# Kernel tuning notes

Measured on AMD Instinct MI355X. Metric: run time of the kernel, lower is better.

Reference implementation:

```python
import jax, jax.numpy as jnp
import numpy as np

# GCN ('gcn' variant): avg-pooled adjacency, per-step linear + propagation + ReLU,
# final output projection, then select the target (first) node of each block.
# The original builds a dense block-diagonal (B*n, B*n) adjacency via torch.block_diag;
# since off-block entries are exactly zero, this is mathematically identical to
# batched per-block matmuls, which is what we do here.

B, N_NODES, D_IN, D_HID, D_OUT, STEPS = 256, 512, 256, 256, 128, 3


def setup_inputs() -> dict:
    key = jax.random.key(0)
    ks = jax.random.split(key, 6)
    xavier = lambda k, shp: jax.random.normal(k, shp, jnp.float32) * np.sqrt(2.0 / (shp[0] + shp[1]))
    feat = jax.random.normal(ks[0], (B * N_NODES, D_IN), jnp.float32)
    raw_adj = jax.random.uniform(ks[1], (B, N_NODES, N_NODES), jnp.float32)
    W0 = xavier(ks[2], (D_IN, D_HID))
    W1 = xavier(ks[3], (D_HID, D_HID))
    W2 = xavier(ks[4], (D_HID, D_HID))
    Wout = xavier(ks[5], (D_HID, D_OUT))
    return {"feat": feat, "raw_adj": raw_adj, "W0": W0, "W1": W1, "W2": W2, "Wout": Wout}


def reference(feat, raw_adj, W0, W1, W2, Wout):
    b, n, _ = raw_adj.shape
    d = feat.shape[1]
    Xb = feat.reshape(b, n, d)  # block view of feat

    # avg_pooling: row-normalize adjacency by the sum over columns whose
    # feature rows are nonzero (block-diagonal => per-block computation).
    nz = (jnp.linalg.norm(Xb, axis=2) > 0).astype(raw_adj.dtype)  # (b, n)
    row_sum = jnp.einsum('bij,bj->bi', raw_adj, nz)               # (b, n)
    row_sum = jnp.where(row_sum == 0, 1.0, row_sum)
    adj = raw_adj / row_sum[:, :, None]

    X = Xb
    for W in (W0, W1, W2):
        Z = jnp.einsum('bnd,dh->bnh', X, W)      # per-step linear (no bias)
        X = jax.nn.relu(jnp.einsum('bij,bjh->bih', adj, Z))  # propagate + ReLU
    out = jnp.einsum('bnh,ho->bno', X, Wout)     # output layer
    # X[ids] with ids = [0, n, 2n, ...] == first node of each block
    return out[:, 0, :]
```

## Files before the change

### kernel.cpp

```cpp
#include <hip/hip_runtime.h>


typedef __attribute__((ext_vector_type(8))) short short8;
typedef __attribute__((ext_vector_type(4))) float f32x4;

__device__ __forceinline__ unsigned short f2bf(float x) {
  unsigned u = __float_as_uint(x);
  unsigned r = u + 0x7fffu + ((u >> 16) & 1u);
  return (unsigned short)(r >> 16);
}
__device__ __forceinline__ float bf2f(unsigned short b) {
  return __uint_as_float(((unsigned)b) << 16);
}

#define GLDS(g, l) __builtin_amdgcn_global_load_lds( \
    (const __attribute__((address_space(1))) void*)(g), \
    (__attribute__((address_space(3))) void*)(l), 16, 0, 0)

__global__ void k_feat(const float* __restrict__ feat,
                       unsigned short* __restrict__ Xb,
                       float* __restrict__ nz) {
  int row = blockIdx.x * 4 + (threadIdx.x >> 6);
  int lane = threadIdx.x & 63;
  float4 v = ((const float4*)feat)[(size_t)row * 64 + lane];
  float ssq = v.x * v.x + v.y * v.y + v.z * v.z + v.w * v.w;
#pragma unroll
  for (int off = 1; off < 64; off <<= 1) ssq += __shfl_xor(ssq, off);
  if (lane == 0) nz[row] = (ssq > 0.f) ? 1.f : 0.f;
  ushort4 p;
  p.x = f2bf(v.x); p.y = f2bf(v.y); p.z = f2bf(v.z); p.w = f2bf(v.w);
  ((ushort4*)Xb)[(size_t)row * 64 + lane] = p;
}

__global__ void k_adj(const float* __restrict__ adj, const float* __restrict__ nz,
                      unsigned short* __restrict__ adjN) {
  int row = blockIdx.x * 4 + (threadIdx.x >> 6);
  int lane = threadIdx.x & 63;
  int b = row >> 9;
  const float4* src = (const float4*)(adj + (size_t)row * 512);
  float4 a0 = src[lane * 2], a1 = src[lane * 2 + 1];
  const float4* nzp = (const float4*)(nz + (size_t)b * 512);
  float4 z0 = nzp[lane * 2], z1 = nzp[lane * 2 + 1];
  float s = a0.x * z0.x + a0.y * z0.y + a0.z * z0.z + a0.w * z0.w
          + a1.x * z1.x + a1.y * z1.y + a1.z * z1.z + a1.w * z1.w;
#pragma unroll
  for (int off = 1; off < 64; off <<= 1) s += __shfl_xor(s, off);
  float inv = 1.f / ((s == 0.f) ? 1.f : s);
  uint4 p;
  p.x = (unsigned)f2bf(a0.x * inv) | ((unsigned)f2bf(a0.y * inv) << 16);
  p.y = (unsigned)f2bf(a0.z * inv) | ((unsigned)f2bf(a0.w * inv) << 16);
  p.z = (unsigned)f2bf(a1.x * inv) | ((unsigned)f2bf(a1.y * inv) << 16);
  p.w = (unsigned)f2bf(a1.z * inv) | ((unsigned)f2bf(a1.w * inv) << 16);
  ((uint4*)(adjN + (size_t)row * 512))[lane] = p;
}

__global__ void k_wconv(const float* __restrict__ W0, const float* __restrict__ W1,
                        unsigned short* __restrict__ Wt) {
  int s = blockIdx.x >> 8;
  int n = blockIdx.x & 255;
  int k = threadIdx.x;
  const float* W = s ? W1 : W0;
  Wt[(size_t)s * 65536 + n * 256 + k] = f2bf(W[(size_t)k * 256 + n]);
}

__device__ __forceinline__ void gemm_tile(
    const char* Ag, int ldaB, const char* Bg, int ldbB, int nkt,
    char* ldsA, char* ldsB, f32x4 acc[4][4], int wm, int wn, int lane, int tid) {
  for (int kt = 0; kt < nkt; ++kt) {
#pragma unroll
    for (int q = 0; q < 4; ++q) {
      int P = (q * 256 + tid) * 16;
      int L = P ^ (((P >> 7) & 7) << 4);
      int row = L >> 7, cb = L & 127;
      GLDS(Ag + (size_t)row * ldaB + kt * 128 + cb, ldsA + P);
      GLDS(Bg + (size_t)row * ldbB + kt * 128 + cb, ldsB + P);
    }
    __syncthreads();
#pragma unroll
    for (int ks = 0; ks < 2; ++ks) {
      short8 af[4], bfr[4];
      int c = ks * 64 + ((lane >> 4) << 4);
#pragma unroll
      for (int m = 0; m < 4; ++m) {
        int row = wm * 64 + m * 16 + (lane & 15);
        af[m] = *(const short8*)(ldsA + ((row * 128 + c) ^ ((row & 7) << 4)));
      }
#pragma unroll
      for (int n = 0; n < 4; ++n) {
        int row = wn * 64 + n * 16 + (lane & 15);
        bfr[n] = *(const short8*)(ldsB + ((row * 128 + c) ^ ((row & 7) << 4)));
      }
#pragma unroll
      for (int m = 0; m < 4; ++m)
#pragma unroll
        for (int n = 0; n < 4; ++n)
          acc[m][n] = __builtin_amdgcn_mfma_f32_16x16x32_bf16(af[m], bfr[n], acc[m][n], 0, 0, 0);
    }
    __syncthreads();
  }
}

__device__ __forceinline__ int swz2048(int bid) {
  return (bid & 7) * 256 + (bid >> 3);
}

__global__ __launch_bounds__(256) void k_linear(const unsigned short* __restrict__ X,
                                                const unsigned short* __restrict__ Wt,
                                                unsigned short* __restrict__ Zt) {
  __shared__ char lds[32768];
  int tid = threadIdx.x, lane = tid & 63, wid = tid >> 6;
  int wm = wid >> 1, wn = wid & 1;
  int tile = swz2048(blockIdx.x);
  int tm = tile >> 1, tn = tile & 1;
  const char* Ag = (const char*)(X + (size_t)tm * 128 * 256);
  const char* Bg = (const char*)(Wt + (size_t)tn * 128 * 256);
  f32x4 acc[4][4];
#pragma unroll
  for (int m = 0; m < 4; ++m)
#pragma unroll
    for (int n = 0; n < 4; ++n) { f32x4 z = {0.f, 0.f, 0.f, 0.f}; acc[m][n] = z; }
  gemm_tile(Ag, 512, Bg, 512, 4, lds, lds + 16384, acc, wm, wn, lane, tid);
  int b = tm >> 2;
  int node_base = ((tm & 3) * 128) + wm * 64;
  int h_base = tn * 128 + wn * 64;
#pragma unroll
  for (int m = 0; m < 4; ++m) {
    int node = node_base + m * 16 + ((lane >> 4) << 2);
#pragma unroll
    for (int n = 0; n < 4; ++n) {
      int h = h_base + n * 16 + (lane & 15);
      f32x4 v = acc[m][n];
      ushort4 p;
      p.x = f2bf(v[0]); p.y = f2bf(v[1]); p.z = f2bf(v[2]); p.w = f2bf(v[3]);
      *(ushort4*)(Zt + ((size_t)b * 256 + h) * 512 + node) = p;
    }
  }
}

__global__ __launch_bounds__(256) void k_prop(const unsigned short* __restrict__ adjN,
                                              const unsigned short* __restrict__ Zt,
                                              unsigned short* __restrict__ Xout) {
  __shared__ char lds[32768];
  int tid = threadIdx.x, lane = tid & 63, wid = tid >> 6;
  int wm = wid >> 1, wn = wid & 1;
  int tile = swz2048(blockIdx.x);
  int b = tile >> 3, tm = (tile >> 1) & 3, tn = tile & 1;
  const char* Ag = (const char*)(adjN + ((size_t)b * 512 + tm * 128) * 512);
  const char* Bg = (const char*)(Zt + ((size_t)b * 256 + tn * 128) * 512);
  f32x4 acc[4][4];
#pragma unroll
  for (int m = 0; m < 4; ++m)
#pragma unroll
    for (int n = 0; n < 4; ++n) { f32x4 z = {0.f, 0.f, 0.f, 0.f}; acc[m][n] = z; }
  gemm_tile(Ag, 1024, Bg, 1024, 8, lds, lds + 16384, acc, wm, wn, lane, tid);
  int node_base = tm * 128 + wm * 64;
  int h_base = tn * 128 + wn * 64;
#pragma unroll
  for (int m = 0; m < 4; ++m) {
    int node = node_base + m * 16 + ((lane >> 4) << 2);
#pragma unroll
    for (int n = 0; n < 4; ++n) {
      int h = h_base + n * 16 + (lane & 15);
#pragma unroll
      for (int r = 0; r < 4; ++r) {
        float v = acc[m][n][r];
        v = v > 0.f ? v : 0.f;
        Xout[((size_t)b * 512 + node + r) * 256 + h] = f2bf(v);
      }
    }
  }
}

__global__ __launch_bounds__(256) void k_tail(const unsigned short* __restrict__ adjN,
                                              const unsigned short* __restrict__ X2,
                                              const float* __restrict__ W2,
                                              const float* __restrict__ Wout,
                                              float* __restrict__ out) {
  __shared__ float aL[512];
  __shared__ float yL[8][256];
  __shared__ float y[256];
  __shared__ float x3[256];
  int b = blockIdx.x, tid = threadIdx.x;
  {
    const unsigned short* a0 = adjN + (size_t)b * 512 * 512;
    ushort2 v = ((const ushort2*)a0)[tid];
    aL[tid * 2] = bf2f(v.x);
    aL[tid * 2 + 1] = bf2f(v.y);
  }
  __syncthreads();
  {
    int hg = tid & 31, jg = tid >> 5;
    float acc[8] = {0.f, 0.f, 0.f, 0.f, 0.f, 0.f, 0.f, 0.f};
    const unsigned short* Xb = X2 + (size_t)b * 512 * 256;
    for (int jj = 0; jj < 64; ++jj) {
      int j = jj * 8 + jg;
      short8 xv = *(const short8*)(Xb + (size_t)j * 256 + hg * 8);
      float a = aL[j];
#pragma unroll
      for (int r = 0; r < 8; ++r) acc[r] += a * bf2f((unsigned short)xv[r]);
    }
#pragma unroll
    for (int r = 0; r < 8; ++r) yL[jg][hg * 8 + r] = acc[r];
  }
  __syncthreads();
  {
    float s = 0.f;
#pragma unroll
    for (int g = 0; g < 8; ++g) s += yL[g][tid];
    y[tid] = s;
  }
  __syncthreads();
  {
    float s = 0.f;
    for (int k = 0; k < 256; ++k) s += y[k] * W2[(size_t)k * 256 + tid];
    x3[tid] = s > 0.f ? s : 0.f;
  }
  __syncthreads();
  if (tid < 128) {
    float s = 0.f;
    for (int h = 0; h < 256; ++h) s += x3[h] * Wout[(size_t)h * 128 + tid];
    out[(size_t)b * 128 + tid] = s;
  }
}

extern "C" void kernel_launch(void* const* d_in, const int* in_sizes, int n_in,
                              void* d_out, int out_size, void* d_ws, size_t ws_size,
                              hipStream_t stream) {
  (void)in_sizes; (void)n_in; (void)out_size; (void)ws_size;
  const float* feat = (const float*)d_in[0];
  const float* adj  = (const float*)d_in[1];
  const float* W0   = (const float*)d_in[2];
  const float* W1   = (const float*)d_in[3];
  const float* W2   = (const float*)d_in[4];
  const float* Wout = (const float*)d_in[5];
  float* out = (float*)d_out;

  char* ws = (char*)d_ws;
  unsigned short* adjN = (unsigned short*)(ws);
  unsigned short* Xbuf = (unsigned short*)(ws + 134217728);
  unsigned short* Zt   = (unsigned short*)(ws + 201326592);
  float* nzbuf         = (float*)(ws + 268435456);
  unsigned short* Wt   = (unsigned short*)(ws + 268959744);

  k_feat<<<32768, 256, 0, stream>>>(feat, Xbuf, nzbuf);
  k_adj<<<32768, 256, 0, stream>>>(adj, nzbuf, adjN);
  k_wconv<<<512, 256, 0, stream>>>(W0, W1, Wt);

  k_linear<<<2048, 256, 0, stream>>>(Xbuf, Wt, Zt);
  k_prop<<<2048, 256, 0, stream>>>(adjN, Zt, Xbuf);
  k_linear<<<2048, 256, 0, stream>>>(Xbuf, Wt + 65536, Zt);
  k_prop<<<2048, 256, 0, stream>>>(adjN, Zt, Xbuf);
  k_tail<<<256, 256, 0, stream>>>(adjN, Xbuf, W2, Wout, out);
}
```

Measured before the change: 347.5 us.

## Fuse feature/adjacency conversion into GEMMs and compute row sums via MFMA

Removes the separate feat and adjacency preprocessing kernels. The first linear layer now reads fp32 features directly, converts them to bf16 in registers and writes the nonzero mask as a side output. The propagation kernel reads raw fp32 adjacency, converts it on the fly and computes row sums with an extra MFMA against the bf16 nz vector, applying the normalization in the epilogue. The bf16 adjN buffer write and re-read go away, but the fp32 adjacency (twice the bytes of bf16) is now read on each of the two propagation passes and in the tail, and A-tile loads become synchronous register loads instead of async global-to-LDS copies.

```diff
diff --git a/kernel.cpp b/kernel.cpp
--- a/kernel.cpp
+++ b/kernel.cpp
@@ -12,46 +12,18 @@
 __device__ __forceinline__ float bf2f(unsigned short b) {
   return __uint_as_float(((unsigned)b) << 16);
 }
+__device__ __forceinline__ unsigned pkbf(float lo, float hi) {
+  unsigned r;
+  asm("v_cvt_pk_bf16_f32 %0, %1, %2" : "=v"(r) : "v"(lo), "v"(hi));
+  return r;
+}
 
 #define GLDS(g, l) __builtin_amdgcn_global_load_lds( \
     (const __attribute__((address_space(1))) void*)(g), \
     (__attribute__((address_space(3))) void*)(l), 16, 0, 0)
 
-__global__ void k_feat(const float* __restrict__ feat,
-                       unsigned short* __restrict__ Xb,
-                       float* __restrict__ nz) {
-  int row = blockIdx.x * 4 + (threadIdx.x >> 6);
-  int lane = threadIdx.x & 63;
-  float4 v = ((const float4*)feat)[(size_t)row * 64 + lane];
-  float ssq = v.x * v.x + v.y * v.y + v.z * v.z + v.w * v.w;
-#pragma unroll
-  for (int off = 1; off < 64; off <<= 1) ssq += __shfl_xor(ssq, off);
-  if (lane == 0) nz[row] = (ssq > 0.f) ? 1.f : 0.f;
-  ushort4 p;
-  p.x = f2bf(v.x); p.y = f2bf(v.y); p.z = f2bf(v.z); p.w = f2bf(v.w);
-  ((ushort4*)Xb)[(size_t)row * 64 + lane] = p;
-}
-
-__global__ void k_adj(const float* __restrict__ adj, const float* __restrict__ nz,
-                      unsigned short* __restrict__ adjN) {
-  int row = blockIdx.x * 4 + (threadIdx.x >> 6);
-  int lane = threadIdx.x & 63;
-  int b = row >> 9;
-  const float4* src = (const float4*)(adj + (size_t)row * 512);
-  float4 a0 = src[lane * 2], a1 = src[lane * 2 + 1];
-  const float4* nzp = (const float4*)(nz + (size_t)b * 512);
-  float4 z0 = nzp[lane * 2], z1 = nzp[lane * 2 + 1];
-  float s = a0.x * z0.x + a0.y * z0.y + a0.z * z0.z + a0.w * z0.w
-          + a1.x * z1.x + a1.y * z1.y + a1.z * z1.z + a1.w * z1.w;
-#pragma unroll
-  for (int off = 1; off < 64; off <<= 1) s += __shfl_xor(s, off);
-  float inv = 1.f / ((s == 0.f) ? 1.f : s);
-  uint4 p;
-  p.x = (unsigned)f2bf(a0.x * inv) | ((unsigned)f2bf(a0.y * inv) << 16);
-  p.y = (unsigned)f2bf(a0.z * inv) | ((unsigned)f2bf(a0.w * inv) << 16);
-  p.z = (unsigned)f2bf(a1.x * inv) | ((unsigned)f2bf(a1.y * inv) << 16);
-  p.w = (unsigned)f2bf(a1.z * inv) | ((unsigned)f2bf(a1.w * inv) << 16);
-  ((uint4*)(adjN + (size_t)row * 512))[lane] = p;
+__device__ __forceinline__ int swz2048(int bid) {
+  return (bid & 7) * 256 + (bid >> 3);
 }
 
 __global__ void k_wconv(const float* __restrict__ W0, const float* __restrict__ W1,
@@ -100,8 +72,195 @@
   }
 }
 
-__device__ __forceinline__ int swz2048(int bid) {
-  return (bid & 7) * 256 + (bid >> 3);
+__global__ __launch_bounds__(256) void k_lin0(const float* __restrict__ feat,
+                                              const unsigned short* __restrict__ Wt,
+                                              unsigned short* __restrict__ Zt,
+                                              float* __restrict__ nzOut) {
+  __shared__ char ldsA[16384];
+  __shared__ char ldsB[16384];
+  int tid = threadIdx.x, lane = tid & 63, wid = tid >> 6;
+  int wm = wid >> 1, wn = wid & 1;
+  int tile = swz2048(blockIdx.x);
+  int tm = tile >> 1, tn = tile & 1;
+  const float* Ag = feat + (size_t)tm * 128 * 256;
+  const char* Bg = (const char*)(Wt + (size_t)tn * 128 * 256);
+  int r = tid >> 1, hk = tid & 1;
+  const float* myrow = Ag + (size_t)r * 256 + hk * 32;
+  float ssq = 0.f;
+  f32x4 acc[4][4];
+#pragma unroll
+  for (int m = 0; m < 4; ++m)
+#pragma unroll
+    for (int n = 0; n < 4; ++n) { f32x4 z = {0.f, 0.f, 0.f, 0.f}; acc[m][n] = z; }
+
+  for (int kt = 0; kt < 4; ++kt) {
+#pragma unroll
+    for (int q = 0; q < 4; ++q) {
+      int P = (q * 256 + tid) * 16;
+      int L = P ^ (((P >> 7) & 7) << 4);
+      int row = L >> 7, cb = L & 127;
+      GLDS(Bg + (size_t)row * 512 + kt * 128 + cb, ldsB + P);
+    }
+    float4 f[8];
+#pragma unroll
+    for (int q = 0; q < 8; ++q) f[q] = ((const float4*)(myrow + kt * 64))[q];
+#pragma unroll
+    for (int q = 0; q < 8; ++q)
+      ssq += f[q].x * f[q].x + f[q].y * f[q].y + f[q].z * f[q].z + f[q].w * f[q].w;
+#pragma unroll
+    for (int q = 0; q < 4; ++q) {
+      uint4 w;
+      w.x = pkbf(f[2 * q].x, f[2 * q].y);
+      w.y = pkbf(f[2 * q].z, f[2 * q].w);
+      w.z = pkbf(f[2 * q + 1].x, f[2 * q + 1].y);
+      w.w = pkbf(f[2 * q + 1].z, f[2 * q + 1].w);
+      int cb = hk * 64 + q * 16;
+      *(uint4*)(ldsA + ((r * 128 + cb) ^ ((r & 7) << 4))) = w;
+    }
+    __syncthreads();
+#pragma unroll
+    for (int ks = 0; ks < 2; ++ks) {
+      short8 af[4], bfr[4];
+      int c = ks * 64 + ((lane >> 4) << 4);
+#pragma unroll
+      for (int m = 0; m < 4; ++m) {
+        int row = wm * 64 + m * 16 + (lane & 15);
+        af[m] = *(const short8*)(ldsA + ((row * 128 + c) ^ ((row & 7) << 4)));
+      }
+#pragma unroll
+      for (int n = 0; n < 4; ++n) {
+        int row = wn * 64 + n * 16 + (lane & 15);
+        bfr[n] = *(const short8*)(ldsB + ((row * 128 + c) ^ ((row & 7) << 4)));
+      }
+#pragma unroll
+      for (int m = 0; m < 4; ++m)
+#pragma unroll
+        for (int n = 0; n < 4; ++n)
+          acc[m][n] = __builtin_amdgcn_mfma_f32_16x16x32_bf16(af[m], bfr[n], acc[m][n], 0, 0, 0);
+    }
+    __syncthreads();
+  }
+
+  float tot = ssq + __shfl_xor(ssq, 1);
+  if (hk == 0 && tn == 0) nzOut[(size_t)tm * 128 + r] = (tot > 0.f) ? 1.f : 0.f;
+
+  int b = tm >> 2;
+  int node_base = ((tm & 3) * 128) + wm * 64;
+  int h_base = tn * 128 + wn * 64;
+#pragma unroll
+  for (int m = 0; m < 4; ++m) {
+    int node = node_base + m * 16 + ((lane >> 4) << 2);
+#pragma unroll
+    for (int n = 0; n < 4; ++n) {
+      int h = h_base + n * 16 + (lane & 15);
+      f32x4 v = acc[m][n];
+      ushort4 p;
+      p.x = f2bf(v[0]); p.y = f2bf(v[1]); p.z = f2bf(v[2]); p.w = f2bf(v[3]);
+      *(ushort4*)(Zt + ((size_t)b * 256 + h) * 512 + node) = p;
+    }
+  }
+}
+
+__global__ __launch_bounds__(256) void k_propf(const float* __restrict__ adj,
+                                               const unsigned short* __restrict__ Zt,
+                                               const float* __restrict__ nz,
+                                               unsigned short* __restrict__ Xout) {
+  __shared__ char ldsA[16384];
+  __shared__ char ldsB[16384];
+  __shared__ char nzbfL[1024];
+  int tid = threadIdx.x, lane = tid & 63, wid = tid >> 6;
+  int wm = wid >> 1, wn = wid & 1;
+  int tile = swz2048(blockIdx.x);
+  int b = tile >> 3, tm = (tile >> 1) & 3, tn = tile & 1;
+  const float* Ag = adj + ((size_t)b * 512 + tm * 128) * 512;
+  const char* Bg = (const char*)(Zt + ((size_t)b * 256 + tn * 128) * 512);
+  {
+    float2 nv = ((const float2*)(nz + (size_t)b * 512))[tid];
+    ((unsigned*)nzbfL)[tid] = pkbf(nv.x, nv.y);
+  }
+  int r = tid >> 1, hk = tid & 1;
+  const float* myrow = Ag + (size_t)r * 512 + hk * 32;
+  f32x4 acc[4][4];
+  f32x4 acc_rs[4];
+#pragma unroll
+  for (int m = 0; m < 4; ++m) {
+    f32x4 z = {0.f, 0.f, 0.f, 0.f};
+    acc_rs[m] = z;
+#pragma unroll
+    for (int n = 0; n < 4; ++n) acc[m][n] = z;
+  }
+
+  for (int kt = 0; kt < 8; ++kt) {
+#pragma unroll
+    for (int q = 0; q < 4; ++q) {
+      int P = (q * 256 + tid) * 16;
+      int L = P ^ (((P >> 7) & 7) << 4);
+      int row = L >> 7, cb = L & 127;
+      GLDS(Bg + (size_t)row * 1024 + kt * 128 + cb, ldsB + P);
+    }
+    float4 f[8];
+#pragma unroll
+    for (int q = 0; q < 8; ++q) f[q] = ((const float4*)(myrow + kt * 64))[q];
+#pragma unroll
+    for (int q = 0; q < 4; ++q) {
+      uint4 w;
+      w.x = pkbf(f[2 * q].x, f[2 * q].y);
+      w.y = pkbf(f[2 * q].z, f[2 * q].w);
+      w.z = pkbf(f[2 * q + 1].x, f[2 * q + 1].y);
+      w.w = pkbf(f[2 * q + 1].z, f[2 * q + 1].w);
+      int cb = hk * 64 + q * 16;
+      *(uint4*)(ldsA + ((r * 128 + cb) ^ ((r & 7) << 4))) = w;
+    }
+    __syncthreads();
+#pragma unroll
+    for (int ks = 0; ks < 2; ++ks) {
+      short8 af[4], bfr[4], nzf;
+      int c = ks * 64 + ((lane >> 4) << 4);
+      nzf = *(const short8*)(nzbfL + kt * 128 + c);
+#pragma unroll
+      for (int m = 0; m < 4; ++m) {
+        int row = wm * 64 + m * 16 + (lane & 15);
+        af[m] = *(const short8*)(ldsA + ((row * 128 + c) ^ ((row & 7) << 4)));
+      }
+#pragma unroll
+      for (int n = 0; n < 4; ++n) {
+        int row = wn * 64 + n * 16 + (lane & 15);
+        bfr[n] = *(const short8*)(ldsB + ((row * 128 + c) ^ ((row & 7) << 4)));
+      }
+#pragma unroll
+      for (int m = 0; m < 4; ++m)
+        acc_rs[m] = __builtin_amdgcn_mfma_f32_16x16x32_bf16(af[m], nzf, acc_rs[m], 0, 0, 0);
+#pragma unroll
+      for (int m = 0; m < 4; ++m)
+#pragma unroll
+        for (int n = 0; n < 4; ++n)
+          acc[m][n] = __builtin_amdgcn_mfma_f32_16x16x32_bf16(af[m], bfr[n], acc[m][n], 0, 0, 0);
+    }
+    __syncthreads();
+  }
+
+  int node_base = tm * 128 + wm * 64;
+  int h_base = tn * 128 + wn * 64;
+#pragma unroll
+  for (int m = 0; m < 4; ++m) {
+    int node = node_base + m * 16 + ((lane >> 4) << 2);
+    float inv[4];
+#pragma unroll
+    for (int r2 = 0; r2 < 4; ++r2) {
+      float rsv = acc_rs[m][r2];
+      inv[r2] = 1.f / ((rsv == 0.f) ? 1.f : rsv);
+    }
+#pragma unroll
+    for (int n = 0; n < 4; ++n) {
+      int h = h_base + n * 16 + (lane & 15);
+#pragma unroll
+      for (int r2 = 0; r2 < 4; ++r2) {
+        float v = acc[m][n][r2] * inv[r2];
+        v = v > 0.f ? v : 0.f;
+        Xout[((size_t)b * 512 + node + r2) * 256 + h] = f2bf(v);
+      }
+    }
+  }
 }
 
 __global__ __launch_bounds__(256) void k_linear(const unsigned short* __restrict__ X,
@@ -137,77 +296,55 @@
   }
 }
 
-__global__ __launch_bounds__(256) void k_prop(const unsigned short* __restrict__ adjN,
-                                              const unsigned short* __restrict__ Zt,
-                                              unsigned short* __restrict__ Xout) {
-  __shared__ char lds[32768];
-  int tid = threadIdx.x, lane = tid & 63, wid = tid >> 6;
-  int wm = wid >> 1, wn = wid & 1;
-  int tile = swz2048(blockIdx.x);
-  int b = tile >> 3, tm = (tile >> 1) & 3, tn = tile & 1;
-  const char* Ag = (const char*)(adjN + ((size_t)b * 512 + tm * 128) * 512);
-  const char* Bg = (const char*)(Zt + ((size_t)b * 256 + tn * 128) * 512);
-  f32x4 acc[4][4];
-#pragma unroll
-  for (int m = 0; m < 4; ++m)
-#pragma unroll
-    for (int n = 0; n < 4; ++n) { f32x4 z = {0.f, 0.f, 0.f, 0.f}; acc[m][n] = z; }
-  gemm_tile(Ag, 1024, Bg, 1024, 8, lds, lds + 16384, acc, wm, wn, lane, tid);
-  int node_base = tm * 128 + wm * 64;
-  int h_base = tn * 128 + wn * 64;
-#pragma unroll
-  for (int m = 0; m < 4; ++m) {
-    int node = node_base + m * 16 + ((lane >> 4) << 2);
-#pragma unroll
-    for (int n = 0; n < 4; ++n) {
-      int h = h_base + n * 16 + (lane & 15);
-#pragma unroll
-      for (int r = 0; r < 4; ++r) {
-        float v = acc[m][n][r];
-        v = v > 0.f ? v : 0.f;
-        Xout[((size_t)b * 512 + node + r) * 256 + h] = f2bf(v);
-      }
-    }
-  }
-}
-
-__global__ __launch_bounds__(256) void k_tail(const unsigned short* __restrict__ adjN,
+__global__ __launch_bounds__(256) void k_tail(const float* __restrict__ adj,
                                               const unsigned short* __restrict__ X2,
+                                              const float* __restrict__ nz,
                                               const float* __restrict__ W2,
                                               const float* __restrict__ Wout,
                                               float* __restrict__ out) {
   __shared__ float aL[512];
+  __shared__ float red[4];
+  __shared__ float sInv;
   __shared__ float yL[8][256];
   __shared__ float y[256];
   __shared__ float x3[256];
   int b = blockIdx.x, tid = threadIdx.x;
   {
-    const unsigned short* a0 = adjN + (size_t)b * 512 * 512;
-    ushort2 v = ((const ushort2*)a0)[tid];
-    aL[tid * 2] = bf2f(v.x);
-    aL[tid * 2 + 1] = bf2f(v.y);
+    float2 av = ((const float2*)(adj + (size_t)b * 512 * 512))[tid];
+    float2 nv = ((const float2*)(nz + (size_t)b * 512))[tid];
+    aL[2 * tid] = av.x;
+    aL[2 * tid + 1] = av.y;
+    float p = av.x * nv.x + av.y * nv.y;
+#pragma unroll
+    for (int off = 1; off < 64; off <<= 1) p += __shfl_xor(p, off);
+    if ((tid & 63) == 0) red[tid >> 6] = p;
+  }
+  __syncthreads();
+  if (tid == 0) {
+    float s = red[0] + red[1] + red[2] + red[3];
+    sInv = 1.f / ((s == 0.f) ? 1.f : s);
   }
   __syncthreads();
   {
     int hg = tid & 31, jg = tid >> 5;
-    float acc[8] = {0.f, 0.f, 0.f, 0.f, 0.f, 0.f, 0.f, 0.f};
+    float acc8[8] = {0.f, 0.f, 0.f, 0.f, 0.f, 0.f, 0.f, 0.f};
     const unsigned short* Xb = X2 + (size_t)b * 512 * 256;
     for (int jj = 0; jj < 64; ++jj) {
       int j = jj * 8 + jg;
       short8 xv = *(const short8*)(Xb + (size_t)j * 256 + hg * 8);
       float a = aL[j];
 #pragma unroll
-      for (int r = 0; r < 8; ++r) acc[r] += a * bf2f((unsigned short)xv[r]);
-    }
-#pragma unroll
-    for (int r = 0; r < 8; ++r) yL[jg][hg * 8 + r] = acc[r];
+      for (int r = 0; r < 8; ++r) acc8[r] += a * bf2f((unsigned short)xv[r]);
+    }
+#pragma unroll
+    for (int r = 0; r < 8; ++r) yL[jg][hg * 8 + r] = acc8[r];
   }
   __syncthreads();
   {
     float s = 0.f;
 #pragma unroll
     for (int g = 0; g < 8; ++g) s += yL[g][tid];
-    y[tid] = s;
+    y[tid] = s * sInv;
   }
   __syncthreads();
   {
@@ -236,19 +373,16 @@
   float* out = (float*)d_out;
 
   char* ws = (char*)d_ws;
-  unsigned short* adjN = (unsigned short*)(ws);
-  unsigned short* Xbuf = (unsigned short*)(ws + 134217728);
-  unsigned short* Zt   = (unsigned short*)(ws + 201326592);
-  float* nzbuf         = (float*)(ws + 268435456);
-  unsigned short* Wt   = (unsigned short*)(ws + 268959744);
-
-  k_feat<<<32768, 256, 0, stream>>>(feat, Xbuf, nzbuf);
-  k_adj<<<32768, 256, 0, stream>>>(adj, nzbuf, adjN);
+  unsigned short* Xbuf = (unsigned short*)(ws);
+  unsigned short* Zt   = (unsigned short*)(ws + 67108864);
+  float* nzbuf         = (float*)(ws + 134217728);
+  unsigned short* Wt   = (unsigned short*)(ws + 134742016);
+
   k_wconv<<<512, 256, 0, stream>>>(W0, W1, Wt);
 
-  k_linear<<<2048, 256, 0, stream>>>(Xbuf, Wt, Zt);
-  k_prop<<<2048, 256, 0, stream>>>(adjN, Zt, Xbuf);
+  k_lin0<<<2048, 256, 0, stream>>>(feat, Wt, Zt, nzbuf);
+  k_propf<<<2048, 256, 0, stream>>>(adj, Zt, nzbuf, Xbuf);
   k_linear<<<2048, 256, 0, stream>>>(Xbuf, Wt + 65536, Zt);
-  k_prop<<<2048, 256, 0, stream>>>(adjN, Zt, Xbuf);
-  k_tail<<<256, 256, 0, stream>>>(adjN, Xbuf, W2, Wout, out);
-}
+  k_propf<<<2048, 256, 0, stream>>>(adj, Zt, nzbuf, Xbuf);
+  k_tail<<<256, 256, 0, stream>>>(adj, Xbuf, nzbuf, W2, Wout, out);
+}
```

Result: slower. 408.5 us (+17.5%).
